# Optimization experiments

Hardware: AMD Instinct MI355X
Metric: run time of the kernel (lower is better)

Reference implementation:

```python
import jax, jax.numpy as jnp
import numpy as np

NUM_SAMPLE = 10   # self._num, hard-coded as range(10) in prob_sample
FSCALE = 5        # neighbor-count kernel
CSCALE = 3        # constraint-count kernel
EPS = 1e-16


def _sum_window(x, k):
    # x: [N,H,W] -> SAME-padded k x k box sum == F.conv2d with ones(1,1,k,k), padding=(k-1)//2
    return jax.lax.reduce_window(x, 0.0, jax.lax.add, (1, k, k), (1, 1, 1), 'SAME')


def _dilate8(x):
    # 3x3 max-pool = one step of 8-connectivity dilation (skimage flood_fill default
    # connectivity for 2D is full connectivity when my_connectivity is None)
    return jax.lax.reduce_window(x, 0.0, jax.lax.max, (1, 3, 3), (1, 1, 1), 'SAME')


def _flood_fill(fg, seed_r, seed_c):
    # fg: [N,H,W] binary float; returns the fg-connected component containing the seed,
    # via fixed-point iteration of masked dilation (equivalent to skimage.flood_fill
    # seeded at the max-neighbor pixel, then thresholding the filled value).
    N, H, W = fg.shape
    reach0 = jnp.zeros_like(fg).at[jnp.arange(N), seed_r, seed_c].set(1.0) * fg

    def cond(st):
        _, changed, it = st
        return changed & (it < H * W)

    def body(st):
        reach, _, it = st
        new = jnp.maximum(reach, _dilate8(reach) * fg)
        return new, jnp.any(new > reach), it + 1

    reach, _, _ = jax.lax.while_loop(cond, body, (reach0, jnp.array(True), jnp.int32(0)))
    return reach


def connectivity_rewards(sample_ns, fg_num):
    # sample_ns: [n, S, H, W] int class indices. Returns binary rewards [n, S, H, W]
    # (reward_type='binary', run_state='train'). All (image, sample) pairs processed
    # in one batched flood fill per foreground class.
    n, S, H, W = sample_ns.shape
    flat = sample_ns.reshape(n * S, H, W)
    total = jnp.zeros((n * S, H, W), jnp.float32)
    for class_idx in range(1, fg_num):  # small fixed loop over fg classes
        fg = (flat == class_idx).astype(jnp.float32)
        neigh = _sum_window(fg, FSCALE) * fg           # count_neighbor * fg
        neigh_flat = neigh.reshape(n * S, H * W)
        seed = jnp.argmax(neigh_flat, axis=-1)          # pixel with max neighbor count
        has_fg = (jnp.max(neigh_flat, axis=-1) > 0).astype(jnp.float32)
        fill = _flood_fill(fg, seed // W, seed % W) * has_fg[:, None, None]
        Fc = _sum_window(fill, CSCALE) * fill           # F_fg_neigbors
        Sc = _sum_window(fg, CSCALE) * fg               # S_fg_neigbors
        r = (jnp.where(Fc == 0, -1.0, Fc) == jnp.where(Sc == 0, -2.0, Sc)).astype(jnp.float32)
        total = total + r
    return total.reshape(n, S, H, W)


def setup_inputs() -> dict:
    key = jax.random.key(0)
    logits = jax.random.normal(key, (4, 4, 512, 512), dtype=jnp.float32)
    preds = jax.nn.softmax(logits, axis=1)  # per-pixel class probabilities [n,c,h,w]
    return {"preds": preds}


def reference(preds):
    n, c, h, w = preds.shape
    skey = jax.random.key(42)
    # prob_sample: per-pixel multinomial over classes, repeated NUM_SAMPLE times
    lg = jnp.moveaxis(jnp.log(preds + EPS), 1, -1)  # [n,h,w,c]
    samp = jax.random.categorical(skey, lg, axis=-1, shape=(NUM_SAMPLE, n, h, w))
    sample_ns = jnp.transpose(samp, (1, 0, 2, 3)).astype(jnp.int32)  # [n,S,h,w]
    prob_ns = jnp.take_along_axis(preds, sample_ns, axis=1)          # [n,S,h,w]
    rewards = jax.lax.stop_gradient(connectivity_rewards(sample_ns, c))
    # REINFORCE objective: maximize reward-weighted log-prob of sampled labelings
    loss = -(rewards * jnp.log(prob_ns + EPS)).mean()
    return loss
```

## Files before the change

kernel.cpp:

```cpp
#include <hip/hip_runtime.h>
#include <stdint.h>

#define SNUM 10
#define NBATCH 4
#define NCLS 4
#define HH 512
#define WW 512
#define IMG (HH*WW)
#define NPIX (SNUM*NBATCH*IMG)
#define WPI (IMG/32)
#define QCAP 3584

__device__ __forceinline__ float u01(uint32_t bits) {
  const float f = __uint_as_float((bits >> 9) | 0x3f800000u) - 1.0f;
  return fmaxf(f, 1.17549435e-38f);
}

__device__ __forceinline__ uint32_t unpack32(uint64_t v) {
  uint64_t tt = v | (v >> 1);
  uint64_t u = ~tt & 0x5555555555555555ULL;
  u = (u ^ (u >> 1))  & 0x3333333333333333ULL;
  u = (u ^ (u >> 2))  & 0x0F0F0F0F0F0F0F0FULL;
  u = (u ^ (u >> 4))  & 0x00FF00FF00FF00FFULL;
  u = (u ^ (u >> 8))  & 0x0000FFFF0000FFFFULL;
  u = (u ^ (u >> 16)) & 0x00000000FFFFFFFFULL;
  return (uint32_t)u;
}

__global__ __launch_bounds__(256) void k_sample(const float* __restrict__ preds,
                                                uint8_t* __restrict__ packed,
                                                float* __restrict__ acc,
                                                uint32_t* __restrict__ gkey,
                                                uint32_t* __restrict__ misc) {
  const int t = blockIdx.x * 256 + threadIdx.x;
  if (t == 0) acc[0] = 0.0f;
  if (t < 120) gkey[t] = 0u;
  if (t == 120) misc[0] = 0u;
  const int sn = t >> 16;
  const int n  = sn & 3;
  const int pg = t & 65535;
  const int pix = pg << 2;

  float pp[NCLS][4];
#pragma unroll
  for (int c = 0; c < NCLS; ++c) {
    const float4 v = *reinterpret_cast<const float4*>(
        preds + (((int64_t)(n * NCLS + c)) << 18) + pix);
    pp[c][0] = v.x; pp[c][1] = v.y; pp[c][2] = v.z; pp[c][3] = v.w;
  }

  const uint32_t gb = (uint32_t)sn * 1048576u + ((uint32_t)pix << 2);
  const uint32_t k1 = 42u;
  const uint32_t k2 = 42u ^ 0x1BD11BDAu;
  uint32_t byte = 0;

#define TFR4(r) { \
  _Pragma("unroll") \
  for (int c_ = 0; c_ < 4; ++c_) { \
    x0[c_] += x1[c_]; \
    const uint32_t xr_ = x1[c_]; \
    x1[c_] = ((xr_ << (r)) | (xr_ >> (32 - (r)))) ^ x0[c_]; \
  } }
#define INJ4(a, b) { \
  _Pragma("unroll") \
  for (int c_ = 0; c_ < 4; ++c_) { x0[c_] += (a); x1[c_] += (b); } }

#pragma unroll
  for (int j = 0; j < 4; ++j) {
    uint32_t x0[4], x1[4];
#pragma unroll
    for (int c = 0; c < 4; ++c) {
      x0[c] = 0u;
      x1[c] = gb + (uint32_t)(4 * j + c) + k1;
    }
    TFR4(13) TFR4(15) TFR4(26) TFR4(6)
    INJ4(k1, k2 + 1u)
    TFR4(17) TFR4(29) TFR4(16) TFR4(24)
    INJ4(k2, 2u)
    TFR4(13) TFR4(15) TFR4(26) TFR4(6)
    INJ4(0u, k1 + 3u)
    TFR4(17) TFR4(29) TFR4(16) TFR4(24)
    INJ4(k1, k2 + 4u)
    TFR4(13) TFR4(15) TFR4(26) TFR4(6)
    float lg[4];
#pragma unroll
    for (int c = 0; c < 4; ++c)
      lg[c] = __log2f(u01((x0[c] + k2) ^ (x1[c] + 5u)));

    float bp = pp[0][j];
    float bl = lg[0];
    int bc = 0;
#pragma unroll
    for (int c = 1; c < NCLS; ++c) {
      if (pp[c][j] * bl < bp * lg[c]) { bp = pp[c][j]; bl = lg[c]; bc = c; }
    }
    byte |= (uint32_t)bc << (2 * j);
  }
#undef TFR4
#undef INJ4
  packed[t] = (uint8_t)byte;
}

__global__ __launch_bounds__(256) void k_argmax(const uint8_t* __restrict__ packed,
                                                uint32_t* __restrict__ gkey) {
  __shared__ uint32_t sfg[36 * 16];
  __shared__ uint32_t skey;
  const int tid = threadIdx.x;
  const int b = blockIdx.x;
  const int prob = b >> 4;
  const int slab = b & 15;
  const int sn = prob % 40;
  const int k  = 1 + prob / 40;
  if (tid == 0) skey = 0u;

  const uint64_t* p64 = reinterpret_cast<const uint64_t*>(packed);
  const uint64_t pat = (uint64_t)k * 0x5555555555555555ULL;
  const int gr0 = slab * 32 - 2;
  for (int wi = tid; wi < 36 * 16; wi += 256) {
    const int gr = gr0 + (wi >> 4);
    uint32_t m = 0;
    if (gr >= 0 && gr < HH)
      m = unpack32(p64[(int64_t)sn * WPI + (gr << 4) + (wi & 15)] ^ pat);
    sfg[wi] = m;
  }
  __syncthreads();

  uint32_t lbest = 0;
  for (int idx = tid; idx < 512; idx += 256) {
    const int rl = 2 + (idx >> 4);
    const int col = idx & 15;
    const uint32_t cw = sfg[(rl << 4) + col];
    if (!cw) continue;
    uint64_t rb[5];
#pragma unroll
    for (int d = 0; d < 5; ++d) {
      const int base = ((rl + d - 2) << 4) + col;
      const uint32_t le = (col > 0)  ? sfg[base - 1] : 0u;
      const uint32_t cu = sfg[base];
      const uint32_t ri = (col < 15) ? sfg[base + 1] : 0u;
      rb[d] = ((uint64_t)(ri & 7u) << 34) | ((uint64_t)cu << 2) | (uint64_t)(le >> 30);
    }
    const int gr = slab * 32 + (idx >> 4);
    uint32_t bits = cw;
    while (bits) {
      const int j = __ffs(bits) - 1;
      bits &= bits - 1;
      int cnt = 0;
#pragma unroll
      for (int d = 0; d < 5; ++d)
        cnt += __popc((uint32_t)(rb[d] >> j) & 0x1fu);
      const uint32_t fidx = (uint32_t)((gr << 9) + (col << 5) + j);
      const uint32_t key = ((uint32_t)cnt << 18) | (0x3FFFFu - fidx);
      lbest = lbest > key ? lbest : key;
    }
  }
#pragma unroll
  for (int off = 32; off > 0; off >>= 1) {
    const uint32_t o = (uint32_t)__shfl_down((int)lbest, off, 64);
    lbest = lbest > o ? lbest : o;
  }
  if ((threadIdx.x & 63) == 0 && lbest) atomicMax(&skey, lbest);
  __syncthreads();
  if (tid == 0 && skey) atomicMax(&gkey[prob], skey);
}


__device__ __forceinline__ uint32_t runmask(uint32_t m, uint32_t s) {
  uint32_t out = 0;
  while (s) {
    const int j = __ffs(s) - 1;
    const uint32_t bj = 1u << j;
    const uint32_t up = ((m + bj) ^ m) & m;
    const uint32_t rm = __brev(m);
    const uint32_t rbj = 1u << (31 - j);
    const uint32_t dn = __brev(((rm + rbj) ^ rm) & rm);
    const uint32_t run = up | dn;
    out |= run;
    s &= ~run;
  }
  return out;
}

__device__ __forceinline__ void claimf(uint32_t* fg, uint32_t* qw, uint32_t* qb,
                                       uint32_t* qtail, uint32_t t, uint32_t want) {
  const uint32_t old = atomicAnd(&fg[t], ~want);
  uint32_t nb = old & want;
  if (!nb) return;
  const uint32_t ext = runmask(old, nb) & ~nb;
  if (ext) {
    const uint32_t old2 = atomicAnd(&fg[t], ~ext);
    nb |= old2 & ext;
  }
  const uint32_t slot = atomicAdd(qtail, 1u);
  if (slot < QCAP) { qw[slot] = t; qb[slot] = nb; }
}

__device__ __forceinline__ uint64_t shup64(uint64_t v) {
  const uint32_t lo = __shfl_up((unsigned int)v, 1, 64);
  const uint32_t hi = __shfl_up((unsigned int)(v >> 32), 1, 64);
  return ((uint64_t)hi << 32) | lo;
}
__device__ __forceinline__ uint64_t shdn64(uint64_t v) {
  const uint32_t lo = __shfl_down((unsigned int)v, 1, 64);
  const uint32_t hi = __shfl_down((unsigned int)(v >> 32), 1, 64);
  return ((uint64_t)hi << 32) | lo;
}

__global__ __launch_bounds__(256) void k_fill(const float* __restrict__ preds,
                                              const uint8_t* __restrict__ packed,
                                              const uint32_t* __restrict__ gkey,
                                              uint32_t* __restrict__ misc,
                                              float* __restrict__ acc,
                                              float* __restrict__ out) {
  __shared__ uint32_t fg[WPI];
  __shared__ uint32_t qw[QCAP];
  __shared__ uint32_t qb[QCAP];
  __shared__ uint32_t qtail;
  __shared__ uint32_t sfb;
  __shared__ uint32_t stail;
  __shared__ float    sred[4];
  const int tid = threadIdx.x;
  const int prob = blockIdx.x;
  const int sn = prob % 40;
  const int k  = 1 + prob / 40;
  const int n  = sn & 3;
  uint32_t* filldone = misc + 0;

  if (tid == 0) { sfb = 0u; qtail = 0u; }
  __syncthreads();

  const uint32_t bkey = gkey[prob];
  const uint32_t seed = 0x3FFFFu - (bkey & 0x3FFFFu);
  const float* chan = preds + (((int64_t)n) * NCLS + k) * (int64_t)IMG;
  const uint64_t* p64 = reinterpret_cast<const uint64_t*>(packed);
  const uint64_t pat = (uint64_t)k * 0x5555555555555555ULL;
  float local = 0.0f;

  if ((bkey >> 18) != 0u) {
    if (tid < 64) {
      const int sr = (int)(seed >> 9), sc = (int)(seed & 511);
      int r0 = sr - 31; if (r0 < 0) r0 = 0; if (r0 > HH - 64) r0 = HH - 64;
      int cl = (sc >> 5) - (((sc & 31) < 16) ? 1 : 0);
      if (cl < 0) cl = 0; if (cl > 14) cl = 14;
      const int ar = r0 + tid;
      const int64_t pb = (int64_t)sn * WPI + (ar << 4) + cl;
      const uint64_t fgw = ((uint64_t)unpack32(p64[pb + 1] ^ pat) << 32)
                         |            unpack32(p64[pb]     ^ pat);
      const uint64_t rfg = __brevll(fgw);
      uint64_t fill = (ar == sr) ? (1ULL << (sc - (cl << 5))) : 0ULL;

      bool conv = false;
      for (int it = 0; it < 2048; ++it) {
        uint64_t up = shup64(fill); if (tid == 0)  up = 0ULL;
        uint64_t dn = shdn64(fill); if (tid == 63) dn = 0ULL;
        const uint64_t sp = fill | up | dn;
        uint64_t s = fgw & (sp | (sp << 1) | (sp >> 1));
        uint64_t nf = 0ULL;
        while (s) {
          const int j = __ffsll((unsigned long long)s) - 1;
          const uint64_t upr = ((fgw + (1ULL << j)) ^ fgw) & fgw;
          const uint64_t dnr = __brevll(((rfg + (1ULL << (63 - j))) ^ rfg) & rfg);
          const uint64_t run = upr | dnr;
          nf |= run;
          s &= ~run;
        }
        const bool ch = (nf != fill);
        fill = nf;
        if (__ballot(ch) == 0ULL) { conv = true; break; }
      }

      bool esc = !conv;
      if (fill) {
        if (tid == 0 && r0 > 0) esc = true;
        if (tid == 63 && r0 + 63 < HH - 1) esc = true;
        if ((fill & 1ULL) && cl > 0) esc = true;
        if ((fill >> 63) && cl < 14) esc = true;
      }

      if (__ballot(esc) == 0ULL) {
        uint64_t bits = fill;
        const float* rowp = chan + (int64_t)ar * WW + (cl << 5);
        while (bits) {
          const int j = __ffsll((unsigned long long)bits) - 1;
          bits &= bits - 1;
          local += logf(rowp[j] + 1e-16f);
        }
      } else if (tid == 0) {
        sfb = 1u;
      }
    }
    __syncthreads();

    if (sfb) {
      for (int wi = tid; wi < WPI; wi += 256)
        fg[wi] = unpack32(p64[(int64_t)sn * WPI + wi] ^ pat);
      __syncthreads();
      claimf(fg, qw, qb, &qtail, seed >> 5, 1u << (seed & 31));
      uint32_t head = 0;
      while (true) {
        __syncthreads();
        if (tid == 0) { uint32_t tl = qtail; stail = tl > QCAP ? QCAP : tl; }
        __syncthreads();
        const uint32_t tail = stail;
        if (head >= tail) break;
        for (uint32_t i = head + (uint32_t)tid; i < tail; i += 256) {
          const uint32_t w = qw[i], got = qb[i];
          const int row = (int)(w >> 4), cb = (int)(w & 15);
          const uint32_t spread = got | (got << 1) | (got >> 1);
          const bool lo = (got & 1u) != 0u, hi = (got >> 31) != 0u;
          if (row > 0) {
            claimf(fg, qw, qb, &qtail, w - 16, spread);
            if (cb > 0 && lo)  claimf(fg, qw, qb, &qtail, w - 17, 0x80000000u);
            if (cb < 15 && hi) claimf(fg, qw, qb, &qtail, w - 15, 1u);
          }
          if (row < HH - 1) {
            claimf(fg, qw, qb, &qtail, w + 16, spread);
            if (cb > 0 && lo)  claimf(fg, qw, qb, &qtail, w + 15, 0x80000000u);
            if (cb < 15 && hi) claimf(fg, qw, qb, &qtail, w + 17, 1u);
          }
          if (cb > 0 && lo)  claimf(fg, qw, qb, &qtail, w - 1, 0x80000000u);
          if (cb < 15 && hi) claimf(fg, qw, qb, &qtail, w + 1, 1u);
        }
        head = tail;
      }
      const uint32_t tot = stail;
      for (uint32_t i = (uint32_t)tid; i < tot; i += 256) {
        const uint32_t w = qw[i];
        uint32_t bits = qb[i];
        const int row = (int)(w >> 4);
        const int colb = (int)(w & 15) << 5;
        const float* rowp = chan + (int64_t)row * WW;
        while (bits) {
          const int j = __ffs(bits) - 1;
          bits &= bits - 1;
          local += logf(rowp[colb + j] + 1e-16f);
        }
      }
    }
  }

#pragma unroll
  for (int off = 32; off > 0; off >>= 1)
    local += __shfl_down(local, off, 64);
  if ((tid & 63) == 0) sred[tid >> 6] = local;
  __syncthreads();
  if (tid == 0) {
    const float tot = sred[0] + sred[1] + sred[2] + sred[3];
    if (tot != 0.0f) atomicAdd(acc, tot);
    __threadfence();
    const uint32_t old = atomicAdd(filldone, 1u);
    if (old == 119u) {
      const float s = atomicAdd(acc, 0.0f);
      out[0] = -s / 10485760.0f;
    }
  }
}

extern "C" void kernel_launch(void* const* d_in, const int* in_sizes, int n_in,
                              void* d_out, int out_size, void* d_ws, size_t ws_size,
                              hipStream_t stream) {
  const float* preds = (const float*)d_in[0];
  float* out = (float*)d_out;
  char* ws = (char*)d_ws;
  float*    acc    = (float*)ws;
  uint32_t* gkey   = (uint32_t*)(ws + 64);
  uint32_t* misc   = (uint32_t*)(ws + 1536);
  uint8_t*  packed = (uint8_t*)(ws + 4096);

  k_sample<<<10240, 256, 0, stream>>>(preds, packed, acc, gkey, misc);
  k_argmax<<<1920, 256, 0, stream>>>(packed, gkey);
  k_fill<<<120, 256, 0, stream>>>(preds, packed, gkey, misc, acc, out);
}
```

Baseline: 163.0 us.

## Fuse argmax and flood-fill kernels with last-block-done handoff and global fallback queue

Result: slower. 180.4 us (+10.7%).

```diff
diff --git a/kernel.cpp b/kernel.cpp
--- a/kernel.cpp
+++ b/kernel.cpp
@@ -11,6 +11,8 @@
 #define WPI (IMG/32)
 #define QCAP 3584
 
+#define SCRATCH_OFF (4096 + NPIX/4)
+
 __device__ __forceinline__ float u01(uint32_t bits) {
   const float f = __uint_as_float((bits >> 9) | 0x3f800000u) - 1.0f;
   return fmaxf(f, 1.17549435e-38f);
@@ -35,7 +37,7 @@
   const int t = blockIdx.x * 256 + threadIdx.x;
   if (t == 0) acc[0] = 0.0f;
   if (t < 120) gkey[t] = 0u;
-  if (t == 120) misc[0] = 0u;
+  if (t >= 120 && t < 256) misc[t - 120] = 0u;
   const int sn = t >> 16;
   const int n  = sn & 3;
   const int pg = t & 65535;
@@ -99,69 +101,6 @@
 #undef TFR4
 #undef INJ4
   packed[t] = (uint8_t)byte;
-}
-
-__global__ __launch_bounds__(256) void k_argmax(const uint8_t* __restrict__ packed,
-                                                uint32_t* __restrict__ gkey) {
-  __shared__ uint32_t sfg[36 * 16];
-  __shared__ uint32_t skey;
-  const int tid = threadIdx.x;
-  const int b = blockIdx.x;
-  const int prob = b >> 4;
-  const int slab = b & 15;
-  const int sn = prob % 40;
-  const int k  = 1 + prob / 40;
-  if (tid == 0) skey = 0u;
-
-  const uint64_t* p64 = reinterpret_cast<const uint64_t*>(packed);
-  const uint64_t pat = (uint64_t)k * 0x5555555555555555ULL;
-  const int gr0 = slab * 32 - 2;
-  for (int wi = tid; wi < 36 * 16; wi += 256) {
-    const int gr = gr0 + (wi >> 4);
-    uint32_t m = 0;
-    if (gr >= 0 && gr < HH)
-      m = unpack32(p64[(int64_t)sn * WPI + (gr << 4) + (wi & 15)] ^ pat);
-    sfg[wi] = m;
-  }
-  __syncthreads();
-
-  uint32_t lbest = 0;
-  for (int idx = tid; idx < 512; idx += 256) {
-    const int rl = 2 + (idx >> 4);
-    const int col = idx & 15;
-    const uint32_t cw = sfg[(rl << 4) + col];
-    if (!cw) continue;
-    uint64_t rb[5];
-#pragma unroll
-    for (int d = 0; d < 5; ++d) {
-      const int base = ((rl + d - 2) << 4) + col;
-      const uint32_t le = (col > 0)  ? sfg[base - 1] : 0u;
-      const uint32_t cu = sfg[base];
-      const uint32_t ri = (col < 15) ? sfg[base + 1] : 0u;
-      rb[d] = ((uint64_t)(ri & 7u) << 34) | ((uint64_t)cu << 2) | (uint64_t)(le >> 30);
-    }
-    const int gr = slab * 32 + (idx >> 4);
-    uint32_t bits = cw;
-    while (bits) {
-      const int j = __ffs(bits) - 1;
-      bits &= bits - 1;
-      int cnt = 0;
-#pragma unroll
-      for (int d = 0; d < 5; ++d)
-        cnt += __popc((uint32_t)(rb[d] >> j) & 0x1fu);
-      const uint32_t fidx = (uint32_t)((gr << 9) + (col << 5) + j);
-      const uint32_t key = ((uint32_t)cnt << 18) | (0x3FFFFu - fidx);
-      lbest = lbest > key ? lbest : key;
-    }
-  }
-#pragma unroll
-  for (int off = 32; off > 0; off >>= 1) {
-    const uint32_t o = (uint32_t)__shfl_down((int)lbest, off, 64);
-    lbest = lbest > o ? lbest : o;
-  }
-  if ((threadIdx.x & 63) == 0 && lbest) atomicMax(&skey, lbest);
-  __syncthreads();
-  if (tid == 0 && skey) atomicMax(&gkey[prob], skey);
 }
 
 
@@ -192,7 +131,7 @@
     nb |= old2 & ext;
   }
   const uint32_t slot = atomicAdd(qtail, 1u);
-  if (slot < QCAP) { qw[slot] = t; qb[slot] = nb; }
+  if (slot < QCAP) { atomicExch(&qw[slot], t); atomicExch(&qb[slot], nb); }
 }
 
 __device__ __forceinline__ uint64_t shup64(uint64_t v) {
@@ -206,34 +145,98 @@
   return ((uint64_t)hi << 32) | lo;
 }
 
-__global__ __launch_bounds__(256) void k_fill(const float* __restrict__ preds,
-                                              const uint8_t* __restrict__ packed,
-                                              const uint32_t* __restrict__ gkey,
-                                              uint32_t* __restrict__ misc,
-                                              float* __restrict__ acc,
-                                              float* __restrict__ out) {
-  __shared__ uint32_t fg[WPI];
-  __shared__ uint32_t qw[QCAP];
-  __shared__ uint32_t qb[QCAP];
-  __shared__ uint32_t qtail;
+__global__ __launch_bounds__(256) void k_af(const float* __restrict__ preds,
+                                            const uint8_t* __restrict__ packed,
+                                            uint32_t* __restrict__ gkey,
+                                            uint32_t* __restrict__ misc,
+                                            float* __restrict__ acc,
+                                            float* __restrict__ out,
+                                            uint32_t* __restrict__ scratch) {
+  __shared__ uint32_t sfg[36 * 16];
+  __shared__ uint32_t skey;
+  __shared__ uint32_t sfin;
+  __shared__ uint32_t sbk;
   __shared__ uint32_t sfb;
   __shared__ uint32_t stail;
   __shared__ float    sred[4];
   const int tid = threadIdx.x;
-  const int prob = blockIdx.x;
+  const int b = blockIdx.x;
+  const int prob = b >> 4;
+  const int slab = b & 15;
   const int sn = prob % 40;
   const int k  = 1 + prob / 40;
   const int n  = sn & 3;
-  uint32_t* filldone = misc + 0;
-
-  if (tid == 0) { sfb = 0u; qtail = 0u; }
+  if (tid == 0) skey = 0u;
+
+  const uint64_t* p64 = reinterpret_cast<const uint64_t*>(packed);
+  const uint64_t pat = (uint64_t)k * 0x5555555555555555ULL;
+
+  const int gr0 = slab * 32 - 2;
+  for (int wi = tid; wi < 36 * 16; wi += 256) {
+    const int gr = gr0 + (wi >> 4);
+    uint32_t m = 0;
+    if (gr >= 0 && gr < HH)
+      m = unpack32(p64[(int64_t)sn * WPI + (gr << 4) + (wi & 15)] ^ pat);
+    sfg[wi] = m;
+  }
   __syncthreads();
 
-  const uint32_t bkey = gkey[prob];
+  uint32_t lbest = 0;
+  for (int idx = tid; idx < 512; idx += 256) {
+    const int rl = 2 + (idx >> 4);
+    const int col = idx & 15;
+    const uint32_t cw = sfg[(rl << 4) + col];
+    if (!cw) continue;
+    uint64_t rb[5];
+#pragma unroll
+    for (int d = 0; d < 5; ++d) {
+      const int base = ((rl + d - 2) << 4) + col;
+      const uint32_t le = (col > 0)  ? sfg[base - 1] : 0u;
+      const uint32_t cu = sfg[base];
+      const uint32_t ri = (col < 15) ? sfg[base + 1] : 0u;
+      rb[d] = ((uint64_t)(ri & 7u) << 34) | ((uint64_t)cu << 2) | (uint64_t)(le >> 30);
+    }
+    const int gr = slab * 32 + (idx >> 4);
+    uint32_t bits = cw;
+    while (bits) {
+      const int j = __ffs(bits) - 1;
+      bits &= bits - 1;
+      int cnt = 0;
+#pragma unroll
+      for (int d = 0; d < 5; ++d)
+        cnt += __popc((uint32_t)(rb[d] >> j) & 0x1fu);
+      const uint32_t fidx = (uint32_t)((gr << 9) + (col << 5) + j);
+      const uint32_t key = ((uint32_t)cnt << 18) | (0x3FFFFu - fidx);
+      lbest = lbest > key ? lbest : key;
+    }
+  }
+#pragma unroll
+  for (int off = 32; off > 0; off >>= 1) {
+    const uint32_t o = (uint32_t)__shfl_down((int)lbest, off, 64);
+    lbest = lbest > o ? lbest : o;
+  }
+  if ((tid & 63) == 0 && lbest) atomicMax(&skey, lbest);
+  __syncthreads();
+
+  if (tid == 0) {
+    if (skey) atomicMax(&gkey[prob], skey);
+    __threadfence();
+    const uint32_t a = atomicAdd(&misc[8 + prob], 1u);
+    uint32_t f = 0u;
+    if (a == 15u) { f = 1u; sbk = atomicAdd(&gkey[prob], 0u); }
+    sfin = f;
+    sfb = 0u;
+  }
+  __syncthreads();
+  if (!sfin) return;
+
+  uint32_t* qtail = scratch;
+  uint32_t* fgg   = scratch + 16;
+  uint32_t* qw    = scratch + 16 + WPI;
+  uint32_t* qb    = scratch + 16 + WPI + QCAP;
+  const uint32_t bkey = sbk;
   const uint32_t seed = 0x3FFFFu - (bkey & 0x3FFFFu);
   const float* chan = preds + (((int64_t)n) * NCLS + k) * (int64_t)IMG;
-  const uint64_t* p64 = reinterpret_cast<const uint64_t*>(packed);
-  const uint64_t pat = (uint64_t)k * 0x5555555555555555ULL;
   float local = 0.0f;
 
   if ((bkey >> 18) != 0u) {
@@ -292,41 +295,47 @@
     __syncthreads();
 
     if (sfb) {
+      if (tid == 0) {
+        const uint32_t tk = atomicAdd(&misc[1], 1u);
+        while (atomicAdd(&misc[2], 0u) != tk) __builtin_amdgcn_s_sleep(32);
+        atomicExch(qtail, 0u);
+      }
+      __syncthreads();
       for (int wi = tid; wi < WPI; wi += 256)
-        fg[wi] = unpack32(p64[(int64_t)sn * WPI + wi] ^ pat);
+        atomicExch(&fgg[wi], unpack32(p64[(int64_t)sn * WPI + wi] ^ pat));
       __syncthreads();
-      claimf(fg, qw, qb, &qtail, seed >> 5, 1u << (seed & 31));
+      claimf(fgg, qw, qb, qtail, seed >> 5, 1u << (seed & 31));
       uint32_t head = 0;
       while (true) {
         __syncthreads();
-        if (tid == 0) { uint32_t tl = qtail; stail = tl > QCAP ? QCAP : tl; }
+        if (tid == 0) { uint32_t tl = atomicAdd(qtail, 0u); stail = tl > QCAP ? QCAP : tl; }
         __syncthreads();
         const uint32_t tail = stail;
         if (head >= tail) break;
         for (uint32_t i = head + (uint32_t)tid; i < tail; i += 256) {
-          const uint32_t w = qw[i], got = qb[i];
+          const uint32_t w = atomicAdd(&qw[i], 0u), got = atomicAdd(&qb[i], 0u);
           const int row = (int)(w >> 4), cb = (int)(w & 15);
           const uint32_t spread = got | (got << 1) | (got >> 1);
           const bool lo = (got & 1u) != 0u, hi = (got >> 31) != 0u;
           if (row > 0) {
-            claimf(fg, qw, qb, &qtail, w - 16, spread);
-            if (cb > 0 && lo)  claimf(fg, qw, qb, &qtail, w - 17, 0x80000000u);
-            if (cb < 15 && hi) claimf(fg, qw, qb, &qtail, w - 15, 1u);
+            claimf(fgg, qw, qb, qtail, w - 16, spread);
+            if (cb > 0 && lo)  claimf(fgg, qw, qb, qtail, w - 17, 0x80000000u);
+            if (cb < 15 && hi) claimf(fgg, qw, qb, qtail, w - 15, 1u);
           }
           if (row < HH - 1) {
-            claimf(fg, qw, qb, &qtail, w + 16, spread);
-            if (cb > 0 && lo)  claimf(fg, qw, qb, &qtail, w + 15, 0x80000000u);
-            if (cb < 15 && hi) claimf(fg, qw, qb, &qtail, w + 17, 1u);
+            claimf(fgg, qw, qb, qtail, w + 16, spread);
+            if (cb > 0 && lo)  claimf(fgg, qw, qb, qtail, w + 15, 0x80000000u);
+            if (cb < 15 && hi) claimf(fgg, qw, qb, qtail, w + 17, 1u);
           }
-          if (cb > 0 && lo)  claimf(fg, qw, qb, &qtail, w - 1, 0x80000000u);
-          if (cb < 15 && hi) claimf(fg, qw, qb, &qtail, w + 1, 1u);
+          if (cb > 0 && lo)  claimf(fgg, qw, qb, qtail, w - 1, 0x80000000u);
+          if (cb < 15 && hi) claimf(fgg, qw, qb, qtail, w + 1, 1u);
         }
         head = tail;
       }
       const uint32_t tot = stail;
       for (uint32_t i = (uint32_t)tid; i < tot; i += 256) {
-        const uint32_t w = qw[i];
-        uint32_t bits = qb[i];
+        const uint32_t w = atomicAdd(&qw[i], 0u);
+        uint32_t bits = atomicAdd(&qb[i], 0u);
         const int row = (int)(w >> 4);
         const int colb = (int)(w & 15) << 5;
         const float* rowp = chan + (int64_t)row * WW;
@@ -336,6 +345,8 @@
           local += logf(rowp[colb + j] + 1e-16f);
         }
       }
+      __syncthreads();
+      if (tid == 0) atomicAdd(&misc[2], 1u);
     }
   }
 
@@ -348,7 +359,7 @@
     const float tot = sred[0] + sred[1] + sred[2] + sred[3];
     if (tot != 0.0f) atomicAdd(acc, tot);
     __threadfence();
-    const uint32_t old = atomicAdd(filldone, 1u);
+    const uint32_t old = atomicAdd(&misc[0], 1u);
     if (old == 119u) {
       const float s = atomicAdd(acc, 0.0f);
       out[0] = -s / 10485760.0f;
@@ -362,12 +373,12 @@
   const float* preds = (const float*)d_in[0];
   float* out = (float*)d_out;
   char* ws = (char*)d_ws;
-  float*    acc    = (float*)ws;
-  uint32_t* gkey   = (uint32_t*)(ws + 64);
-  uint32_t* misc   = (uint32_t*)(ws + 1536);
-  uint8_t*  packed = (uint8_t*)(ws + 4096);
+  float*    acc     = (float*)ws;
+  uint32_t* gkey    = (uint32_t*)(ws + 64);
+  uint32_t* misc    = (uint32_t*)(ws + 1536);
+  uint8_t*  packed  = (uint8_t*)(ws + 4096);
+  uint32_t* scratch = (uint32_t*)(ws + SCRATCH_OFF);
 
   k_sample<<<10240, 256, 0, stream>>>(preds, packed, acc, gkey, misc);
-  k_argmax<<<1920, 256, 0, stream>>>(packed, gkey);
-  k_fill<<<120, 256, 0, stream>>>(preds, packed, gkey, misc, acc, out);
-}
+  k_af<<<1920, 256, 0, stream>>>(preds, packed, gkey, misc, acc, out, scratch);
+}
```

## Shrink flood-fill block to one wave and add a 128x512 register-tile fallback

Applied to the files above, without the earlier changes.

Measured after the change: 160.4 us. Within noise of the previous version (-1.6%).

```diff
diff --git a/kernel.cpp b/kernel.cpp
--- a/kernel.cpp
+++ b/kernel.cpp
@@ -10,6 +10,7 @@
 #define NPIX (SNUM*NBATCH*IMG)
 #define WPI (IMG/32)
 #define QCAP 3584
+
 
 __device__ __forceinline__ float u01(uint32_t bits) {
   const float f = __uint_as_float((bits >> 9) | 0x3f800000u) - 1.0f;
@@ -181,6 +182,22 @@
   return out;
 }
 
+__device__ __forceinline__ uint64_t runmask64(uint64_t m, uint64_t s) {
+  uint64_t out = 0;
+  while (s) {
+    const int j = __ffsll((unsigned long long)s) - 1;
+    const uint64_t bj = 1ULL << j;
+    const uint64_t up = ((m + bj) ^ m) & m;
+    const uint64_t rm = __brevll(m);
+    const uint64_t rbj = 1ULL << (63 - j);
+    const uint64_t dn = __brevll(((rm + rbj) ^ rm) & rm);
+    const uint64_t run = up | dn;
+    out |= run;
+    s &= ~run;
+  }
+  return out;
+}
+
 __device__ __forceinline__ void claimf(uint32_t* fg, uint32_t* qw, uint32_t* qb,
                                        uint32_t* qtail, uint32_t t, uint32_t want) {
   const uint32_t old = atomicAnd(&fg[t], ~want);
@@ -206,19 +223,16 @@
   return ((uint64_t)hi << 32) | lo;
 }
 
-__global__ __launch_bounds__(256) void k_fill(const float* __restrict__ preds,
-                                              const uint8_t* __restrict__ packed,
-                                              const uint32_t* __restrict__ gkey,
-                                              uint32_t* __restrict__ misc,
-                                              float* __restrict__ acc,
-                                              float* __restrict__ out) {
+__global__ __launch_bounds__(64, 1) void k_fill(const float* __restrict__ preds,
+                                                const uint8_t* __restrict__ packed,
+                                                const uint32_t* __restrict__ gkey,
+                                                uint32_t* __restrict__ misc,
+                                                float* __restrict__ acc,
+                                                float* __restrict__ out) {
   __shared__ uint32_t fg[WPI];
   __shared__ uint32_t qw[QCAP];
   __shared__ uint32_t qb[QCAP];
   __shared__ uint32_t qtail;
-  __shared__ uint32_t sfb;
-  __shared__ uint32_t stail;
-  __shared__ float    sred[4];
   const int tid = threadIdx.x;
   const int prob = blockIdx.x;
   const int sn = prob % 40;
@@ -226,114 +240,186 @@
   const int n  = sn & 3;
   uint32_t* filldone = misc + 0;
 
-  if (tid == 0) { sfb = 0u; qtail = 0u; }
-  __syncthreads();
-
   const uint32_t bkey = gkey[prob];
-  const uint32_t seed = 0x3FFFFu - (bkey & 0x3FFFFu);
-  const float* chan = preds + (((int64_t)n) * NCLS + k) * (int64_t)IMG;
-  const uint64_t* p64 = reinterpret_cast<const uint64_t*>(packed);
-  const uint64_t pat = (uint64_t)k * 0x5555555555555555ULL;
   float local = 0.0f;
-
   if ((bkey >> 18) != 0u) {
-    if (tid < 64) {
-      const int sr = (int)(seed >> 9), sc = (int)(seed & 511);
-      int r0 = sr - 31; if (r0 < 0) r0 = 0; if (r0 > HH - 64) r0 = HH - 64;
-      int cl = (sc >> 5) - (((sc & 31) < 16) ? 1 : 0);
-      if (cl < 0) cl = 0; if (cl > 14) cl = 14;
-      const int ar = r0 + tid;
-      const int64_t pb = (int64_t)sn * WPI + (ar << 4) + cl;
-      const uint64_t fgw = ((uint64_t)unpack32(p64[pb + 1] ^ pat) << 32)
-                         |            unpack32(p64[pb]     ^ pat);
-      const uint64_t rfg = __brevll(fgw);
-      uint64_t fill = (ar == sr) ? (1ULL << (sc - (cl << 5))) : 0ULL;
-
-      bool conv = false;
-      for (int it = 0; it < 2048; ++it) {
-        uint64_t up = shup64(fill); if (tid == 0)  up = 0ULL;
-        uint64_t dn = shdn64(fill); if (tid == 63) dn = 0ULL;
-        const uint64_t sp = fill | up | dn;
-        uint64_t s = fgw & (sp | (sp << 1) | (sp >> 1));
-        uint64_t nf = 0ULL;
-        while (s) {
-          const int j = __ffsll((unsigned long long)s) - 1;
-          const uint64_t upr = ((fgw + (1ULL << j)) ^ fgw) & fgw;
-          const uint64_t dnr = __brevll(((rfg + (1ULL << (63 - j))) ^ rfg) & rfg);
-          const uint64_t run = upr | dnr;
-          nf |= run;
-          s &= ~run;
-        }
-        const bool ch = (nf != fill);
-        fill = nf;
-        if (__ballot(ch) == 0ULL) { conv = true; break; }
+    const uint32_t seed = 0x3FFFFu - (bkey & 0x3FFFFu);
+    const int sr = (int)(seed >> 9), sc = (int)(seed & 511);
+    const float* chan = preds + (((int64_t)n) * NCLS + k) * (int64_t)IMG;
+    const uint64_t* p64 = reinterpret_cast<const uint64_t*>(packed);
+    const uint64_t pat = (uint64_t)k * 0x5555555555555555ULL;
+
+    int r0 = sr - 31; if (r0 < 0) r0 = 0; if (r0 > HH - 64) r0 = HH - 64;
+    int cl = (sc >> 5) - (((sc & 31) < 16) ? 1 : 0);
+    if (cl < 0) cl = 0; if (cl > 14) cl = 14;
+    const int ar = r0 + tid;
+    const int64_t pb = (int64_t)sn * WPI + (ar << 4) + cl;
+    const uint64_t fgw = ((uint64_t)unpack32(p64[pb + 1] ^ pat) << 32)
+                       |            unpack32(p64[pb]     ^ pat);
+    uint64_t fill = (ar == sr) ? (1ULL << (sc - (cl << 5))) : 0ULL;
+
+    bool conv = false;
+    for (int it = 0; it < 256; ++it) {
+      uint64_t up = shup64(fill); if (tid == 0)  up = 0ULL;
+      uint64_t dn = shdn64(fill); if (tid == 63) dn = 0ULL;
+      const uint64_t sp = fill | up | dn;
+      const uint64_t s = fgw & (sp | (sp << 1) | (sp >> 1)) & ~fill;
+      uint64_t nf = fill;
+      if (s) nf |= runmask64(fgw, s);
+      const bool ch = (nf != fill);
+      fill = nf;
+      if (__ballot(ch) == 0ULL) { conv = true; break; }
+    }
+
+    bool esc = !conv;
+    if (fill) {
+      if (tid == 0 && r0 > 0) esc = true;
+      if (tid == 63 && r0 + 63 < HH - 1) esc = true;
+      if ((fill & 1ULL) && cl > 0) esc = true;
+      if ((fill >> 63) && cl < 14) esc = true;
+    }
+
+    if (__ballot(esc) == 0ULL) {
+      uint64_t bits = fill;
+      const float* rowp = chan + (int64_t)ar * WW + (cl << 5);
+      while (bits) {
+        const int j = __ffsll((unsigned long long)bits) - 1;
+        bits &= bits - 1;
+        local += logf(rowp[j] + 1e-16f);
       }
-
-      bool esc = !conv;
-      if (fill) {
-        if (tid == 0 && r0 > 0) esc = true;
-        if (tid == 63 && r0 + 63 < HH - 1) esc = true;
-        if ((fill & 1ULL) && cl > 0) esc = true;
-        if ((fill >> 63) && cl < 14) esc = true;
+    } else {
+      bool done2 = false;
+      {
+        int r0w = sr - 63; if (r0w < 0) r0w = 0; if (r0w > HH - 128) r0w = HH - 128;
+        const int row0 = r0w + 2 * tid;
+        uint64_t fg2[2][8], fl2[2][8];
+#pragma unroll
+        for (int rp = 0; rp < 2; ++rp) {
+          const int64_t base = (int64_t)sn * WPI + ((int64_t)(row0 + rp) << 4);
+#pragma unroll
+          for (int w = 0; w < 8; ++w)
+            fg2[rp][w] = ((uint64_t)unpack32(p64[base + 2 * w + 1] ^ pat) << 32)
+                       |            unpack32(p64[base + 2 * w    ] ^ pat);
+        }
+        const int srp = (sr - r0w) & 1;
+        const int sln = (sr - r0w) >> 1;
+#pragma unroll
+        for (int rp = 0; rp < 2; ++rp)
+#pragma unroll
+          for (int w = 0; w < 8; ++w)
+            fl2[rp][w] = (tid == sln && rp == srp && w == (sc >> 6))
+                         ? (1ULL << (sc & 63)) : 0ULL;
+
+        bool conv2 = false;
+        for (int it = 0; it < 192; ++it) {
+          bool ch = false;
+          uint64_t sp0[8], sp1[8];
+#pragma unroll
+          for (int w = 0; w < 8; ++w) {
+            uint64_t up = shup64(fl2[1][w]); if (tid == 0)  up = 0ULL;
+            uint64_t dn = shdn64(fl2[0][w]); if (tid == 63) dn = 0ULL;
+            sp0[w] = fl2[0][w] | up        | fl2[1][w];
+            sp1[w] = fl2[1][w] | fl2[0][w] | dn;
+          }
+#pragma unroll
+          for (int rp = 0; rp < 2; ++rp) {
+            uint64_t nf[8];
+#pragma unroll
+            for (int w = 0; w < 8; ++w) {
+              const uint64_t spw = rp ? sp1[w] : sp0[w];
+              uint64_t spread = spw | (spw << 1) | (spw >> 1);
+              if (w > 0) spread |= ((rp ? sp1[w-1] : sp0[w-1]) >> 63);
+              if (w < 7) spread |= ((rp ? sp1[w+1] : sp0[w+1]) & 1ULL) << 63;
+              const uint64_t s = spread & fg2[rp][w] & ~fl2[rp][w];
+              nf[w] = fl2[rp][w];
+              if (s) nf[w] |= runmask64(fg2[rp][w], s);
+            }
+#pragma unroll
+            for (int w = 1; w < 8; ++w)
+              if ((nf[w-1] >> 63) && (fg2[rp][w] & 1ULL) && !(nf[w] & 1ULL))
+                nf[w] |= runmask64(fg2[rp][w], 1ULL);
+#pragma unroll
+            for (int w = 6; w >= 0; --w)
+              if ((nf[w+1] & 1ULL) && (fg2[rp][w] >> 63) && !(nf[w] >> 63))
+                nf[w] |= runmask64(fg2[rp][w], 1ULL << 63);
+#pragma unroll
+            for (int w = 0; w < 8; ++w) {
+              ch |= (nf[w] != fl2[rp][w]);
+              fl2[rp][w] = nf[w];
+            }
+          }
+          if (__ballot(ch) == 0ULL) { conv2 = true; break; }
+        }
+
+        bool esc2 = !conv2;
+        {
+          bool any0 = false, any1 = false;
+#pragma unroll
+          for (int w = 0; w < 8; ++w) { any0 |= (fl2[0][w] != 0ULL); any1 |= (fl2[1][w] != 0ULL); }
+          if (tid == 0  && r0w > 0            && any0) esc2 = true;
+          if (tid == 63 && r0w + 127 < HH - 1 && any1) esc2 = true;
+        }
+        if (__ballot(esc2) == 0ULL) {
+          done2 = true;
+#pragma unroll
+          for (int rp = 0; rp < 2; ++rp) {
+            const float* rowp = chan + (int64_t)(row0 + rp) * WW;
+#pragma unroll
+            for (int w = 0; w < 8; ++w) {
+              uint64_t bits = fl2[rp][w];
+              while (bits) {
+                const int j = __ffsll((unsigned long long)bits) - 1;
+                bits &= bits - 1;
+                local += logf(rowp[(w << 6) + j] + 1e-16f);
+              }
+            }
+          }
+        }
       }
 
-      if (__ballot(esc) == 0ULL) {
-        uint64_t bits = fill;
-        const float* rowp = chan + (int64_t)ar * WW + (cl << 5);
-        while (bits) {
-          const int j = __ffsll((unsigned long long)bits) - 1;
-          bits &= bits - 1;
-          local += logf(rowp[j] + 1e-16f);
-        }
-      } else if (tid == 0) {
-        sfb = 1u;
-      }
-    }
-    __syncthreads();
-
-    if (sfb) {
-      for (int wi = tid; wi < WPI; wi += 256)
-        fg[wi] = unpack32(p64[(int64_t)sn * WPI + wi] ^ pat);
-      __syncthreads();
-      claimf(fg, qw, qb, &qtail, seed >> 5, 1u << (seed & 31));
-      uint32_t head = 0;
-      while (true) {
+      if (!done2) {
+        if (tid == 0) qtail = 0u;
+        for (int wi = tid; wi < WPI; wi += 64)
+          fg[wi] = unpack32(p64[(int64_t)sn * WPI + wi] ^ pat);
         __syncthreads();
-        if (tid == 0) { uint32_t tl = qtail; stail = tl > QCAP ? QCAP : tl; }
-        __syncthreads();
-        const uint32_t tail = stail;
-        if (head >= tail) break;
-        for (uint32_t i = head + (uint32_t)tid; i < tail; i += 256) {
-          const uint32_t w = qw[i], got = qb[i];
-          const int row = (int)(w >> 4), cb = (int)(w & 15);
-          const uint32_t spread = got | (got << 1) | (got >> 1);
-          const bool lo = (got & 1u) != 0u, hi = (got >> 31) != 0u;
-          if (row > 0) {
-            claimf(fg, qw, qb, &qtail, w - 16, spread);
-            if (cb > 0 && lo)  claimf(fg, qw, qb, &qtail, w - 17, 0x80000000u);
-            if (cb < 15 && hi) claimf(fg, qw, qb, &qtail, w - 15, 1u);
+        claimf(fg, qw, qb, &qtail, seed >> 5, 1u << (seed & 31));
+        uint32_t head = 0;
+        while (true) {
+          uint32_t tail = atomicAdd(&qtail, 0u);
+          if (tail > QCAP) tail = QCAP;
+          if (head >= tail) break;
+          for (uint32_t i = head + (uint32_t)tid; i < tail; i += 64) {
+            const uint32_t w = qw[i], got = qb[i];
+            const int row = (int)(w >> 4), cb = (int)(w & 15);
+            const uint32_t spread = got | (got << 1) | (got >> 1);
+            const bool lo = (got & 1u) != 0u, hi = (got >> 31) != 0u;
+            if (row > 0) {
+              claimf(fg, qw, qb, &qtail, w - 16, spread);
+              if (cb > 0 && lo)  claimf(fg, qw, qb, &qtail, w - 17, 0x80000000u);
+              if (cb < 15 && hi) claimf(fg, qw, qb, &qtail, w - 15, 1u);
+            }
+            if (row < HH - 1) {
+              claimf(fg, qw, qb, &qtail, w + 16, spread);
+              if (cb > 0 && lo)  claimf(fg, qw, qb, &qtail, w + 15, 0x80000000u);
+              if (cb < 15 && hi) claimf(fg, qw, qb, &qtail, w + 17, 1u);
+            }
+            if (cb > 0 && lo)  claimf(fg, qw, qb, &qtail, w - 1, 0x80000000u);
+            if (cb < 15 && hi) claimf(fg, qw, qb, &qtail, w + 1, 1u);
           }
-          if (row < HH - 1) {
-            claimf(fg, qw, qb, &qtail, w + 16, spread);
-            if (cb > 0 && lo)  claimf(fg, qw, qb, &qtail, w + 15, 0x80000000u);
-            if (cb < 15 && hi) claimf(fg, qw, qb, &qtail, w + 17, 1u);
+          head = tail;
+        }
+        uint32_t tot = qtail; if (tot > QCAP) tot = QCAP;
+        for (uint32_t i = (uint32_t)tid; i < tot; i += 64) {
+          const uint32_t w = qw[i];
+          uint32_t bits = qb[i];
+          const int row = (int)(w >> 4);
+          const int colb = (int)(w & 15) << 5;
+          const float* rowp = chan + (int64_t)row * WW;
+          while (bits) {
+            const int j = __ffs(bits) - 1;
+            bits &= bits - 1;
+            local += logf(rowp[colb + j] + 1e-16f);
           }
-          if (cb > 0 && lo)  claimf(fg, qw, qb, &qtail, w - 1, 0x80000000u);
-          if (cb < 15 && hi) claimf(fg, qw, qb, &qtail, w + 1, 1u);
-        }
-        head = tail;
-      }
-      const uint32_t tot = stail;
-      for (uint32_t i = (uint32_t)tid; i < tot; i += 256) {
-        const uint32_t w = qw[i];
-        uint32_t bits = qb[i];
-        const int row = (int)(w >> 4);
-        const int colb = (int)(w & 15) << 5;
-        const float* rowp = chan + (int64_t)row * WW;
-        while (bits) {
-          const int j = __ffs(bits) - 1;
-          bits &= bits - 1;
-          local += logf(rowp[colb + j] + 1e-16f);
         }
       }
     }
@@ -342,11 +428,8 @@
 #pragma unroll
   for (int off = 32; off > 0; off >>= 1)
     local += __shfl_down(local, off, 64);
-  if ((tid & 63) == 0) sred[tid >> 6] = local;
-  __syncthreads();
   if (tid == 0) {
-    const float tot = sred[0] + sred[1] + sred[2] + sred[3];
-    if (tot != 0.0f) atomicAdd(acc, tot);
+    if (local != 0.0f) atomicAdd(acc, local);
     __threadfence();
     const uint32_t old = atomicAdd(filldone, 1u);
     if (old == 119u) {
@@ -369,5 +452,5 @@
 
   k_sample<<<10240, 256, 0, stream>>>(preds, packed, acc, gkey, misc);
   k_argmax<<<1920, 256, 0, stream>>>(packed, gkey);
-  k_fill<<<120, 256, 0, stream>>>(preds, packed, gkey, misc, acc, out);
-}
+  k_fill<<<120, 64, 0, stream>>>(preds, packed, gkey, misc, acc, out);
+}
```
